# Kernel tuning notes

Hardware: AMD Instinct MI355X
Metric: run time of the kernel (lower is better)

The kernel has to match this reference:

```python
import jax, jax.numpy as jnp
import numpy as np

D, N, P_FULL = 32768, 512, 10
W_SIZES = {0: 8}
P = 8
TRI = P * (P + 1) // 2  # 36


def setup_inputs() -> dict:
    key = jax.random.key(0)
    k1, k2 = jax.random.split(key)
    y = jax.random.uniform(k1, (D, N), dtype=jnp.float32)          # probabilities in (0,1)
    design = jax.random.normal(k2, (D, N, P_FULL), dtype=jnp.float32)
    return {
        "y": y,
        "design": design,
        "inverse_sigmoid_scale": jnp.ones((N,), jnp.float32),
        "h1_weight": jnp.ones((N,), jnp.float32),
        "h1_bias": jnp.zeros((N,), jnp.float32),
        "scale_tril": 10.0 * jnp.ones((D, TRI), jnp.float32),       # init per module: 10*ones
        "regu": -2.0 * jnp.ones((D, P), jnp.float32),               # init per module: -2*ones
        "target_label": 0,
    }


def _forward(y, design, inv_scale, h1_w, h1_b, scale_tril_flat, regu, p):
    # logit transform with clamping, then softplus hidden layer (all elementwise over [D, N])
    yc = jnp.clip(y, 1e-35, 1.0)
    y1m = jnp.clip(1.0 - y, 1e-35, 1.0)
    y_trans = (jnp.log(yc) - jnp.log(y1m)) / 0.1 * inv_scale
    y_trans = y_trans + jax.nn.softplus(y_trans) * h1_w + h1_b

    X = design[..., :p]                                             # [D, N, p]
    # anneal = diag(softplus(regu)) per design: [D, p, p]
    anneal = jax.nn.softplus(regu)[..., None] * jnp.eye(p, dtype=regu.dtype)
    xtx = jnp.einsum('dnp,dnq->dpq', X, X) + anneal                 # [D, p, p]
    xty = jnp.einsum('dnp,dn->dp', X, y_trans)                      # [D, p]
    xtxi = jnp.linalg.inv(xtx)                                      # batched small-matrix inverse
    mu = jnp.einsum('dpq,dq->dp', xtxi, xty)                        # [D, p]

    # fill lower triangle row-major (same order as the torch double loop)
    rows, cols = jnp.tril_indices(p)
    L = jnp.zeros((scale_tril_flat.shape[0], p, p), scale_tril_flat.dtype)
    L = L.at[:, rows, cols].set(scale_tril_flat)                    # [D, p, p]
    return mu, L


def reference(y, design, inverse_sigmoid_scale, h1_weight, h1_bias, scale_tril, regu, target_label):
    p = W_SIZES[int(target_label)]
    return _forward(y, design, inverse_sigmoid_scale, h1_weight, h1_bias, scale_tril, regu, p)
```

## Files before the change

### kernel.cpp

```cpp
#include <hip/hip_runtime.h>

#define DD 32768
#define NN 512
#define PF 10
#define PP 8
#define NACC 44

__device__ __forceinline__ float softplus_f(float x) {
    return fmaxf(x, 0.0f) + log1pf(__expf(-fabsf(x)));
}

__global__ __launch_bounds__(256) void k_sums(
    const float* __restrict__ y,
    const float* __restrict__ design,
    const float* __restrict__ inv_scale,
    const float* __restrict__ h1w,
    const float* __restrict__ h1b,
    float* scratch)
{
    const int lane = threadIdx.x & 63;
    const int d    = blockIdx.x * (blockDim.x >> 6) + (threadIdx.x >> 6);

    float acc[NACC];
#pragma unroll
    for (int k = 0; k < NACC; ++k) acc[k] = 0.0f;

    const float2* dp = (const float2*)(design + (size_t)d * (NN * PF));
    const float*  yp = y + (size_t)d * NN;

#pragma unroll 1
    for (int i = 0; i < NN / 64; ++i) {
        const int n  = i * 64 + lane;
        const int r5 = n * 5;
        float2 a0 = dp[r5 + 0];
        float2 a1 = dp[r5 + 1];
        float2 a2 = dp[r5 + 2];
        float2 a3 = dp[r5 + 3];
        const float X[8] = {a0.x, a0.y, a1.x, a1.y, a2.x, a2.y, a3.x, a3.y};

        float yv = yp[n];
        float yc = fminf(fmaxf(yv, 1e-35f), 1.0f);
        float ym = fminf(fmaxf(1.0f - yv, 1e-35f), 1.0f);
        float t  = (__logf(yc) - __logf(ym)) * 10.0f * inv_scale[n];
        float yt = fmaf(softplus_f(t), h1w[n], t) + h1b[n];

        int k = 0;
#pragma unroll
        for (int p = 0; p < PP; ++p) {
#pragma unroll
            for (int q = 0; q <= p; ++q, ++k) acc[k] = fmaf(X[p], X[q], acc[k]);
        }
#pragma unroll
        for (int p = 0; p < PP; ++p) acc[36 + p] = fmaf(X[p], yt, acc[36 + p]);
    }

#pragma unroll
    for (int off = 32; off; off >>= 1) {
#pragma unroll
        for (int k = 0; k < NACC; ++k) acc[k] += __shfl_xor(acc[k], off, 64);
    }

    if (lane == 0) {
        float4* o = (float4*)(scratch + (size_t)d * 64);
#pragma unroll
        for (int k = 0; k < 11; ++k)
            o[k] = make_float4(acc[4 * k], acc[4 * k + 1], acc[4 * k + 2], acc[4 * k + 3]);
    }
}

__global__ __launch_bounds__(256) void k_solve(
    const float* regu_,
    const float* scale_tril_,
    float* out)
{
    const int d = blockIdx.x * blockDim.x + threadIdx.x;
    const float* __restrict__ regu       = regu_;
    const float* __restrict__ scale_tril = scale_tril_;
    float* mu_out = out;
    float* Lreg   = out + (size_t)DD * 8;

    float s[NACC];
    {
        const float4* ip = (const float4*)(Lreg + (size_t)d * 64);
#pragma unroll
        for (int k = 0; k < 11; ++k) {
            float4 v = ip[k];
            s[4 * k] = v.x; s[4 * k + 1] = v.y; s[4 * k + 2] = v.z; s[4 * k + 3] = v.w;
        }
    }

    float A[PP][PP];
    {
        int k = 0;
#pragma unroll
        for (int p = 0; p < PP; ++p)
#pragma unroll
            for (int q = 0; q <= p; ++q, ++k) A[p][q] = s[k];
    }
    float b[PP];
#pragma unroll
    for (int p = 0; p < PP; ++p) b[p] = s[36 + p];
#pragma unroll
    for (int p = 0; p < PP; ++p) A[p][p] += softplus_f(regu[(size_t)d * PP + p]);

    float dinv[PP];
#pragma unroll
    for (int j = 0; j < PP; ++j) {
        float v = A[j][j];
#pragma unroll
        for (int k = 0; k < j; ++k) v -= A[j][k] * A[j][k];
        float lj = sqrtf(v);
        float iv = 1.0f / lj;
        A[j][j] = lj;
        dinv[j] = iv;
#pragma unroll
        for (int i = j + 1; i < PP; ++i) {
            float u = A[i][j];
#pragma unroll
            for (int k = 0; k < j; ++k) u -= A[i][k] * A[j][k];
            A[i][j] = u * iv;
        }
    }
    float z[PP];
#pragma unroll
    for (int i = 0; i < PP; ++i) {
        float v = b[i];
#pragma unroll
        for (int k = 0; k < i; ++k) v -= A[i][k] * z[k];
        z[i] = v * dinv[i];
    }
    float m[PP];
#pragma unroll
    for (int i = PP - 1; i >= 0; --i) {
        float v = z[i];
#pragma unroll
        for (int k = i + 1; k < PP; ++k) v -= A[k][i] * m[k];
        m[i] = v * dinv[i];
    }

    {
        float4* om = (float4*)(mu_out + (size_t)d * PP);
        om[0] = make_float4(m[0], m[1], m[2], m[3]);
        om[1] = make_float4(m[4], m[5], m[6], m[7]);
    }

    float st[36];
    {
        const float4* sp = (const float4*)(scale_tril + (size_t)d * 36);
#pragma unroll
        for (int k = 0; k < 9; ++k) {
            float4 v = sp[k];
            st[4 * k] = v.x; st[4 * k + 1] = v.y; st[4 * k + 2] = v.z; st[4 * k + 3] = v.w;
        }
    }
    {
        float4* ol = (float4*)(Lreg + (size_t)d * 64);
#pragma unroll
        for (int r = 0; r < 8; ++r) {
            float row[8];
#pragma unroll
            for (int c = 0; c < 8; ++c)
                row[c] = (c <= r) ? st[(r * (r + 1)) / 2 + c] : 0.0f;
            ol[2 * r + 0] = make_float4(row[0], row[1], row[2], row[3]);
            ol[2 * r + 1] = make_float4(row[4], row[5], row[6], row[7]);
        }
    }
}

extern "C" void kernel_launch(void* const* d_in, const int* in_sizes, int n_in,
                              void* d_out, int out_size, void* d_ws, size_t ws_size,
                              hipStream_t stream) {
    const float* y          = (const float*)d_in[0];
    const float* design     = (const float*)d_in[1];
    const float* inv_scale  = (const float*)d_in[2];
    const float* h1w        = (const float*)d_in[3];
    const float* h1b        = (const float*)d_in[4];
    const float* scale_tril = (const float*)d_in[5];
    const float* regu       = (const float*)d_in[6];

    float* out     = (float*)d_out;
    float* scratch = out + (size_t)DD * 8;

    hipLaunchKernelGGL(k_sums, dim3(DD / 4), dim3(256), 0, stream,
                       y, design, inv_scale, h1w, h1b, scratch);
    hipLaunchKernelGGL(k_solve, dim3(DD / 256), dim3(256), 0, stream,
                       regu, scale_tril, out);
}
```

Baseline: 908.6 us.

## Vectorize design loads two rows per lane, transpose scratch, split L fill kernel

```diff
diff --git a/kernel.cpp b/kernel.cpp
--- a/kernel.cpp
+++ b/kernel.cpp
@@ -2,12 +2,18 @@
 
 #define DD 32768
 #define NN 512
-#define PF 10
 #define PP 8
 #define NACC 44
 
 __device__ __forceinline__ float softplus_f(float x) {
     return fmaxf(x, 0.0f) + log1pf(__expf(-fabsf(x)));
+}
+
+__device__ __forceinline__ float transform_y(float yv, float is, float hw, float hb) {
+    float yc = fminf(fmaxf(yv, 1e-35f), 1.0f);
+    float ym = fminf(fmaxf(1.0f - yv, 1e-35f), 1.0f);
+    float t  = (__logf(yc) - __logf(ym)) * 10.0f * is;
+    return fmaf(softplus_f(t), hw, t) + hb;
 }
 
 __global__ __launch_bounds__(256) void k_sums(
@@ -16,42 +22,54 @@
     const float* __restrict__ inv_scale,
     const float* __restrict__ h1w,
     const float* __restrict__ h1b,
-    float* scratch)
+    float* __restrict__ ws)
 {
     const int lane = threadIdx.x & 63;
-    const int d    = blockIdx.x * (blockDim.x >> 6) + (threadIdx.x >> 6);
+    const int d    = blockIdx.x * 4 + (threadIdx.x >> 6);
 
     float acc[NACC];
 #pragma unroll
     for (int k = 0; k < NACC; ++k) acc[k] = 0.0f;
 
-    const float2* dp = (const float2*)(design + (size_t)d * (NN * PF));
-    const float*  yp = y + (size_t)d * NN;
+    const float4* dp4 = (const float4*)(design + (size_t)d * (NN * 10));
+    const float2* yp2 = (const float2*)(y + (size_t)d * NN);
+    const float2* is2 = (const float2*)inv_scale;
+    const float2* hw2 = (const float2*)h1w;
+    const float2* hb2 = (const float2*)h1b;
 
 #pragma unroll 1
-    for (int i = 0; i < NN / 64; ++i) {
-        const int n  = i * 64 + lane;
-        const int r5 = n * 5;
-        float2 a0 = dp[r5 + 0];
-        float2 a1 = dp[r5 + 1];
-        float2 a2 = dp[r5 + 2];
-        float2 a3 = dp[r5 + 3];
-        const float X[8] = {a0.x, a0.y, a1.x, a1.y, a2.x, a2.y, a3.x, a3.y};
+    for (int i = 0; i < NN / 128; ++i) {
+        const int m = i * 64 + lane;
+        float4 b0 = dp4[m * 5 + 0];
+        float4 b1 = dp4[m * 5 + 1];
+        float4 b2 = dp4[m * 5 + 2];
+        float4 b3 = dp4[m * 5 + 3];
+        float4 b4 = dp4[m * 5 + 4];
+        float2 yv = yp2[m];
+        float2 is = is2[m];
+        float2 hw = hw2[m];
+        float2 hb = hb2[m];
 
-        float yv = yp[n];
-        float yc = fminf(fmaxf(yv, 1e-35f), 1.0f);
-        float ym = fminf(fmaxf(1.0f - yv, 1e-35f), 1.0f);
-        float t  = (__logf(yc) - __logf(ym)) * 10.0f * inv_scale[n];
-        float yt = fmaf(softplus_f(t), h1w[n], t) + h1b[n];
+        const float X0[8] = {b0.x, b0.y, b0.z, b0.w, b1.x, b1.y, b1.z, b1.w};
+        const float X1[8] = {b2.z, b2.w, b3.x, b3.y, b3.z, b3.w, b4.x, b4.y};
+
+        float yt0 = transform_y(yv.x, is.x, hw.x, hb.x);
+        float yt1 = transform_y(yv.y, is.y, hw.y, hb.y);
 
         int k = 0;
 #pragma unroll
         for (int p = 0; p < PP; ++p) {
 #pragma unroll
-            for (int q = 0; q <= p; ++q, ++k) acc[k] = fmaf(X[p], X[q], acc[k]);
+            for (int q = 0; q <= p; ++q, ++k) {
+                acc[k] = fmaf(X0[p], X0[q], acc[k]);
+                acc[k] = fmaf(X1[p], X1[q], acc[k]);
+            }
         }
 #pragma unroll
-        for (int p = 0; p < PP; ++p) acc[36 + p] = fmaf(X[p], yt, acc[36 + p]);
+        for (int p = 0; p < PP; ++p) {
+            acc[36 + p] = fmaf(X0[p], yt0, acc[36 + p]);
+            acc[36 + p] = fmaf(X1[p], yt1, acc[36 + p]);
+        }
     }
 
 #pragma unroll
@@ -60,34 +78,22 @@
         for (int k = 0; k < NACC; ++k) acc[k] += __shfl_xor(acc[k], off, 64);
     }
 
-    if (lane == 0) {
-        float4* o = (float4*)(scratch + (size_t)d * 64);
+    float myv = 0.0f;
 #pragma unroll
-        for (int k = 0; k < 11; ++k)
-            o[k] = make_float4(acc[4 * k], acc[4 * k + 1], acc[4 * k + 2], acc[4 * k + 3]);
-    }
+    for (int k = 0; k < NACC; ++k) myv = (lane == k) ? acc[k] : myv;
+    if (lane < NACC) ws[(size_t)lane * DD + d] = myv;
 }
 
 __global__ __launch_bounds__(256) void k_solve(
-    const float* regu_,
-    const float* scale_tril_,
-    float* out)
+    const float* __restrict__ ws,
+    const float* __restrict__ regu,
+    float* __restrict__ mu_out)
 {
     const int d = blockIdx.x * blockDim.x + threadIdx.x;
-    const float* __restrict__ regu       = regu_;
-    const float* __restrict__ scale_tril = scale_tril_;
-    float* mu_out = out;
-    float* Lreg   = out + (size_t)DD * 8;
 
     float s[NACC];
-    {
-        const float4* ip = (const float4*)(Lreg + (size_t)d * 64);
 #pragma unroll
-        for (int k = 0; k < 11; ++k) {
-            float4 v = ip[k];
-            s[4 * k] = v.x; s[4 * k + 1] = v.y; s[4 * k + 2] = v.z; s[4 * k + 3] = v.w;
-        }
-    }
+    for (int k = 0; k < NACC; ++k) s[k] = ws[(size_t)k * DD + d];
 
     float A[PP][PP];
     {
@@ -138,33 +144,23 @@
         m[i] = v * dinv[i];
     }
 
-    {
-        float4* om = (float4*)(mu_out + (size_t)d * PP);
-        om[0] = make_float4(m[0], m[1], m[2], m[3]);
-        om[1] = make_float4(m[4], m[5], m[6], m[7]);
-    }
+    float4* om = (float4*)(mu_out + (size_t)d * PP);
+    om[0] = make_float4(m[0], m[1], m[2], m[3]);
+    om[1] = make_float4(m[4], m[5], m[6], m[7]);
+}
 
-    float st[36];
-    {
-        const float4* sp = (const float4*)(scale_tril + (size_t)d * 36);
-#pragma unroll
-        for (int k = 0; k < 9; ++k) {
-            float4 v = sp[k];
-            st[4 * k] = v.x; st[4 * k + 1] = v.y; st[4 * k + 2] = v.z; st[4 * k + 3] = v.w;
-        }
-    }
-    {
-        float4* ol = (float4*)(Lreg + (size_t)d * 64);
-#pragma unroll
-        for (int r = 0; r < 8; ++r) {
-            float row[8];
-#pragma unroll
-            for (int c = 0; c < 8; ++c)
-                row[c] = (c <= r) ? st[(r * (r + 1)) / 2 + c] : 0.0f;
-            ol[2 * r + 0] = make_float4(row[0], row[1], row[2], row[3]);
-            ol[2 * r + 1] = make_float4(row[4], row[5], row[6], row[7]);
-        }
-    }
+__global__ __launch_bounds__(256) void k_L(
+    const float* __restrict__ scale_tril,
+    float* __restrict__ Lout)
+{
+    const int idx = blockIdx.x * blockDim.x + threadIdx.x;
+    const int d  = idx >> 6;
+    const int rc = idx & 63;
+    const int r  = rc >> 3;
+    const int c  = rc & 7;
+    float v = 0.0f;
+    if (c <= r) v = scale_tril[(size_t)d * 36 + ((r * (r + 1)) >> 1) + c];
+    Lout[idx] = v;
 }
 
 extern "C" void kernel_launch(void* const* d_in, const int* in_sizes, int n_in,
@@ -178,11 +174,13 @@
     const float* scale_tril = (const float*)d_in[5];
     const float* regu       = (const float*)d_in[6];
 
-    float* out     = (float*)d_out;
-    float* scratch = out + (size_t)DD * 8;
+    float* out = (float*)d_out;
+    float* ws  = (float*)d_ws;
 
     hipLaunchKernelGGL(k_sums, dim3(DD / 4), dim3(256), 0, stream,
-                       y, design, inv_scale, h1w, h1b, scratch);
+                       y, design, inv_scale, h1w, h1b, ws);
     hipLaunchKernelGGL(k_solve, dim3(DD / 256), dim3(256), 0, stream,
-                       regu, scale_tril, out);
+                       ws, regu, out);
+    hipLaunchKernelGGL(k_L, dim3(DD * 64 / 256), dim3(256), 0, stream,
+                       scale_tril, out + (size_t)DD * 8);
 }
```

Result: no change. 910.6 us (+0.2%).
